# Optimization experiments

Measured on AMD Instinct MI355X. Metric: run time of the kernel, lower is better.

## Reference

```python
import jax, jax.numpy as jnp
import numpy as np
import math

B, S, E, H = 8, 1024, 512, 8
EPS = 1e-5

def _ln(x, g, b):
    mu = jnp.mean(x, axis=-1, keepdims=True)
    var = jnp.mean(jnp.square(x - mu), axis=-1, keepdims=True)
    return (x - mu) * jax.lax.rsqrt(var + EPS) * g + b

def setup_inputs() -> dict:
    key = jax.random.key(0)
    ks = iter(jax.random.split(key, 40))
    def w(shape, scale=0.02):
        return jax.random.normal(next(ks), shape, dtype=jnp.float32) * scale
    inp = {
        'x': jax.random.normal(next(ks), (B, S, E), dtype=jnp.float32),
        'cond': jax.random.normal(next(ks), (B, 1, E), dtype=jnp.float32),
        # AdaLN modulation linears (stored as (in,out))
        'g1w': w((E, E)), 'g1b': jnp.zeros((E,), jnp.float32),
        'be1w': w((E, E)), 'be1b': jnp.zeros((E,), jnp.float32),
        'a1w': w((E, E)), 'a1b': jnp.zeros((E,), jnp.float32),
        'g2w': w((E, E)), 'g2b': jnp.zeros((E,), jnp.float32),
        'be2w': w((E, E)), 'be2b': jnp.zeros((E,), jnp.float32),
        'a2w': w((E, E)), 'a2b': jnp.zeros((E,), jnp.float32),
        # LayerNorm affine
        'ln1g': jnp.ones((E,), jnp.float32), 'ln1b': jnp.zeros((E,), jnp.float32),
        'ln2g': jnp.ones((E,), jnp.float32), 'ln2b': jnp.zeros((E,), jnp.float32),
        # attention projections: each head has width E -> out dim H*E
        'wq': w((E, H * E)), 'bq': jnp.zeros((H * E,), jnp.float32),
        'wk': w((E, H * E)), 'bk': jnp.zeros((H * E,), jnp.float32),
        'wv': w((E, H * E)), 'bv': jnp.zeros((H * E,), jnp.float32),
        'lvw': w((H * E, E)), 'lvb': jnp.zeros((E,), jnp.float32),
        # FFN
        'f1w': w((E, 4 * E)), 'f1b': jnp.zeros((4 * E,), jnp.float32),
        'f2w': w((4 * E, E)), 'f2b': jnp.zeros((E,), jnp.float32),
    }
    return inp

def reference(x, cond, g1w, g1b, be1w, be1b, a1w, a1b, g2w, g2b, be2w, be2b, a2w, a2b,
              ln1g, ln1b, ln2g, ln2b, wq, bq, wk, bk, wv, bv, lvw, lvb, f1w, f1b, f2w, f2b):
    # AdaLN modulation signals, each (B,1,E)
    gamma1 = cond @ g1w + g1b
    beta1 = cond @ be1w + be1b
    alpha1 = cond @ a1w + a1b
    gamma2 = cond @ g2w + g2b
    beta2 = cond @ be2w + be2b
    alpha2 = cond @ a2w + a2b

    y = _ln(x, ln1g, ln1b) * (1.0 + gamma1) + beta1
    q = (y @ wq + bq).reshape(B, S, H, E).transpose(0, 2, 1, 3)  # (B,H,S,E)
    k = (y @ wk + bk).reshape(B, S, H, E).transpose(0, 2, 1, 3)
    v = (y @ wv + bv).reshape(B, S, H, E).transpose(0, 2, 1, 3)
    # NOTE: original scales by sqrt(q.size(2)) == sqrt(seq_len), not head_dim
    scale = 1.0 / math.sqrt(S)
    attn = jax.nn.softmax(jnp.einsum('bhse,bhte->bhst', q, k) * scale, axis=-1)
    o = jnp.einsum('bhst,bhte->bhse', attn, v)  # (B,H,S,E)
    o = o.transpose(0, 2, 1, 3).reshape(B, S, H * E)
    y = x + (o @ lvw + lvb) * alpha1

    z = _ln(y, ln2g, ln2b) * (1.0 + gamma2) + beta2
    z = (jax.nn.relu(z @ f1w + f1b) @ f2w + f2b) * alpha2
    return y + z
```

## Files before the change

### kernel.cpp

```cpp
#include <hip/hip_runtime.h>
#include <hip/hip_bf16.h>

typedef __bf16 bf16_t;
typedef bf16_t bf16x8 __attribute__((ext_vector_type(8)));
typedef bf16_t bf16x4 __attribute__((ext_vector_type(4)));
typedef float f32x4 __attribute__((ext_vector_type(4)));

typedef const __attribute__((address_space(1))) void GV;
typedef __attribute__((address_space(3))) void LV;

__device__ __forceinline__ void gload_lds16(const bf16_t* gsrc, bf16_t* ldst) {
    __builtin_amdgcn_global_load_lds((GV*)gsrc, (LV*)ldst, 16, 0, 0);
}

__global__ __launch_bounds__(256) void wtrans_kernel(const float* __restrict__ in,
                                                     bf16_t* __restrict__ out, int K, int N)
{
    __shared__ float tile[32][33];
    const int n0 = blockIdx.x * 32, k0 = blockIdx.y * 32;
    const int tx = threadIdx.x & 31, ty = threadIdx.x >> 5;
#pragma unroll
    for (int i = 0; i < 32; i += 8)
        tile[ty + i][tx] = in[(long long)(k0 + ty + i) * N + n0 + tx];
    __syncthreads();
#pragma unroll
    for (int i = 0; i < 32; i += 8)
        out[(long long)(n0 + ty + i) * K + k0 + tx] = (bf16_t)tile[tx][ty + i];
}

__global__ __launch_bounds__(256) void modsig_kernel(
    const float* __restrict__ cond,
    const float* __restrict__ w0, const float* __restrict__ w1, const float* __restrict__ w2,
    const float* __restrict__ w3, const float* __restrict__ w4, const float* __restrict__ w5,
    const float* __restrict__ c0, const float* __restrict__ c1, const float* __restrict__ c2,
    const float* __restrict__ c3, const float* __restrict__ c4, const float* __restrict__ c5,
    float* __restrict__ out)
{
    __shared__ float cs[512];
    const int sig = blockIdx.x >> 3, b = blockIdx.x & 7;
    const float* w; const float* bi;
    switch (sig) {
        case 0: w = w0; bi = c0; break;
        case 1: w = w1; bi = c1; break;
        case 2: w = w2; bi = c2; break;
        case 3: w = w3; bi = c3; break;
        case 4: w = w4; bi = c4; break;
        default: w = w5; bi = c5; break;
    }
    for (int i = threadIdx.x; i < 512; i += 256) cs[i] = cond[b * 512 + i];
    __syncthreads();
    for (int n = threadIdx.x; n < 512; n += 256) {
        float s = bi[n];
        for (int i = 0; i < 512; ++i) s = fmaf(cs[i], w[(long long)i * 512 + n], s);
        out[(long long)(sig * 8 + b) * 512 + n] = s;
    }
}

__global__ __launch_bounds__(128) void ln_mod_kernel(
    const float* __restrict__ x, const float* __restrict__ g, const float* __restrict__ be,
    const float* __restrict__ gamma, const float* __restrict__ beta, bf16_t* __restrict__ out)
{
    const int row = blockIdx.x;
    const int b = row >> 10;
    const int t = threadIdx.x;
    const float4 v = reinterpret_cast<const float4*>(x + (long long)row * 512)[t];
    float s = v.x + v.y + v.z + v.w;
    float ss = v.x * v.x + v.y * v.y + v.z * v.z + v.w * v.w;
    for (int o = 32; o; o >>= 1) { s += __shfl_xor(s, o); ss += __shfl_xor(ss, o); }
    __shared__ float red[4];
    if ((t & 63) == 0) { red[t >> 6] = s; red[2 + (t >> 6)] = ss; }
    __syncthreads();
    s = red[0] + red[1]; ss = red[2] + red[3];
    const float mu = s * (1.f / 512.f);
    const float rstd = rsqrtf(ss * (1.f / 512.f) - mu * mu + 1e-5f);
    const float4 gv = reinterpret_cast<const float4*>(g)[t];
    const float4 bv = reinterpret_cast<const float4*>(be)[t];
    const float4 ga = reinterpret_cast<const float4*>(gamma + b * 512)[t];
    const float4 bb = reinterpret_cast<const float4*>(beta + b * 512)[t];
    bf16x4 ov;
    ov[0] = (bf16_t)(((v.x - mu) * rstd * gv.x + bv.x) * (1.f + ga.x) + bb.x);
    ov[1] = (bf16_t)(((v.y - mu) * rstd * gv.y + bv.y) * (1.f + ga.y) + bb.y);
    ov[2] = (bf16_t)(((v.z - mu) * rstd * gv.z + bv.z) * (1.f + ga.z) + bb.z);
    ov[3] = (bf16_t)(((v.w - mu) * rstd * gv.w + bv.w) * (1.f + ga.w) + bb.w);
    reinterpret_cast<bf16x4*>(out + (long long)row * 512)[t] = ov;
}

template <int EPI>
__global__ __launch_bounds__(256) void gemm128_kernel(
    const bf16_t* __restrict__ A, const bf16_t* __restrict__ B,
    const float* __restrict__ bias, void* Cout,
    int M, int N, int K, int lda, int ldb, int ldc)
{
    const int nbx = gridDim.x;
    const int lin = blockIdx.y * nbx + blockIdx.x;
    const int cpx = (nbx * gridDim.y) >> 3;
    const int swz = (lin & 7) * cpx + (lin >> 3);
    const int m0 = (swz / nbx) * 128, n0 = (swz % nbx) * 128;
    const int tid = threadIdx.x, lane = tid & 63, wid = tid >> 6;
    const int wr = wid >> 1, wc = wid & 1;

    __shared__ bf16_t As[8192];
    __shared__ bf16_t Bs[8192];

    f32x4 acc[4][4];
#pragma unroll
    for (int m = 0; m < 4; ++m)
#pragma unroll
        for (int n = 0; n < 4; ++n) acc[m][n] = (f32x4){0.f, 0.f, 0.f, 0.f};

    const int r8 = lane >> 3;
    const int lc = (lane & 7) ^ r8;
    long long aOff[4], bOff[4];
#pragma unroll
    for (int i = 0; i < 4; ++i) {
        const int row = i * 32 + wid * 8 + r8;
        aOff[i] = (long long)(m0 + row) * lda + lc * 8;
        bOff[i] = (long long)(n0 + row) * ldb + lc * 8;
    }

    const int frow = lane & 15, lg = lane >> 4;
    const int p0 = lg ^ (frow & 7);

    for (int kt = 0; kt < K; kt += 64) {
#pragma unroll
        for (int i = 0; i < 4; ++i) gload_lds16(A + aOff[i] + kt, As + i * 2048 + wid * 512);
#pragma unroll
        for (int i = 0; i < 4; ++i) gload_lds16(B + bOff[i] + kt, Bs + i * 2048 + wid * 512);
        __syncthreads();
        __builtin_amdgcn_s_setprio(1);
#pragma unroll
        for (int kk = 0; kk < 2; ++kk) {
            const int pc = p0 ^ (kk << 2);
            bf16x8 af[4], bfv[4];
#pragma unroll
            for (int m = 0; m < 4; ++m)
                af[m] = *reinterpret_cast<const bf16x8*>(As + (wr * 64 + m * 16 + frow) * 64 + pc * 8);
#pragma unroll
            for (int n = 0; n < 4; ++n)
                bfv[n] = *reinterpret_cast<const bf16x8*>(Bs + (wc * 64 + n * 16 + frow) * 64 + pc * 8);
#pragma unroll
            for (int m = 0; m < 4; ++m)
#pragma unroll
                for (int n = 0; n < 4; ++n)
                    acc[m][n] = __builtin_amdgcn_mfma_f32_16x16x32_bf16(af[m], bfv[n], acc[m][n], 0, 0, 0);
        }
        __builtin_amdgcn_s_setprio(0);
        __syncthreads();
    }

#pragma unroll
    for (int m = 0; m < 4; ++m) {
        const int gm = m0 + wr * 64 + m * 16 + ((lane >> 4) << 2);
#pragma unroll
        for (int n = 0; n < 4; ++n) {
            const int gn = n0 + wc * 64 + n * 16 + (lane & 15);
            const float bb = bias ? bias[gn] : 0.f;
#pragma unroll
            for (int j = 0; j < 4; ++j) {
                const float v = acc[m][n][j] + bb;
                const int gmj = gm + j;
                if (EPI == 0) {
                    ((bf16_t*)Cout)[(long long)gmj * ldc + gn] = (bf16_t)v;
                } else {
                    ((bf16_t*)Cout)[(long long)gmj * ldc + gn] = (bf16_t)fmaxf(v, 0.f);
                }
            }
        }
    }
}

__global__ __launch_bounds__(256) void gemmqkv_kernel(
    const bf16_t* __restrict__ A, const bf16_t* __restrict__ B,
    const float* __restrict__ bq, const float* __restrict__ bk, const float* __restrict__ bv,
    bf16_t* __restrict__ qkv, bf16_t* __restrict__ vtb)
{
    const int lin = blockIdx.y * 96 + blockIdx.x;
    const int swz = (lin & 7) * 768 + (lin >> 3);
    const int m0 = (swz / 96) * 128, n0 = (swz % 96) * 128;
    const int sec = n0 >> 12;
    const float* bias = (sec == 0) ? bq : ((sec == 1) ? bk : bv);
    const int tid = threadIdx.x, lane = tid & 63, wid = tid >> 6;
    const int wr = wid >> 1, wc = wid & 1;

    __shared__ bf16_t As[8192];
    __shared__ bf16_t Bs[8192];

    f32x4 acc[4][4];
#pragma unroll
    for (int m = 0; m < 4; ++m)
#pragma unroll
        for (int n = 0; n < 4; ++n) acc[m][n] = (f32x4){0.f, 0.f, 0.f, 0.f};

    const int r8 = lane >> 3;
    const int lc = (lane & 7) ^ r8;
    long long aOff[4], bOff[4];
#pragma unroll
    for (int i = 0; i < 4; ++i) {
        const int row = i * 32 + wid * 8 + r8;
        aOff[i] = (long long)(m0 + row) * 512 + lc * 8;
        bOff[i] = (long long)(n0 + row) * 512 + lc * 8;
    }

    const int frow = lane & 15, lg = lane >> 4;
    const int p0 = lg ^ (frow & 7);

    for (int kt = 0; kt < 512; kt += 64) {
#pragma unroll
        for (int i = 0; i < 4; ++i) gload_lds16(A + aOff[i] + kt, As + i * 2048 + wid * 512);
#pragma unroll
        for (int i = 0; i < 4; ++i) gload_lds16(B + bOff[i] + kt, Bs + i * 2048 + wid * 512);
        __syncthreads();
        __builtin_amdgcn_s_setprio(1);
#pragma unroll
        for (int kk = 0; kk < 2; ++kk) {
            const int pc = p0 ^ (kk << 2);
            bf16x8 af[4], bfv[4];
#pragma unroll
            for (int m = 0; m < 4; ++m)
                af[m] = *reinterpret_cast<const bf16x8*>(As + (wr * 64 + m * 16 + frow) * 64 + pc * 8);
#pragma unroll
            for (int n = 0; n < 4; ++n)
                bfv[n] = *reinterpret_cast<const bf16x8*>(Bs + (wc * 64 + n * 16 + frow) * 64 + pc * 8);
#pragma unroll
            for (int m = 0; m < 4; ++m)
#pragma unroll
                for (int n = 0; n < 4; ++n)
                    acc[m][n] = __builtin_amdgcn_mfma_f32_16x16x32_bf16(af[m], bfv[n], acc[m][n], 0, 0, 0);
        }
        __builtin_amdgcn_s_setprio(0);
        __syncthreads();
    }

#pragma unroll
    for (int m = 0; m < 4; ++m) {
        const int gm = m0 + wr * 64 + m * 16 + ((lane >> 4) << 2);
#pragma unroll
        for (int n = 0; n < 4; ++n) {
            const int gn = n0 + wc * 64 + n * 16 + (lane & 15);
            const int gnl = gn & 4095;
            const float bb = bias[gnl];
#pragma unroll
            for (int j = 0; j < 4; ++j) {
                const float v = acc[m][n][j] + bb;
                const int gmj = gm + j;
                if (sec < 2) {
                    qkv[(long long)sec * 33554432 + (long long)gmj * 4096 + gnl] = (bf16_t)v;
                } else {
                    const long long ci =
                        (long long)(((gmj >> 10) * 8 + (gnl >> 9)) * 512 + (gnl & 511)) * 1024 + (gmj & 1023);
                    vtb[ci] = (bf16_t)v;
                }
            }
        }
    }
}

__global__ __launch_bounds__(256) void gemm64_kernel(
    const bf16_t* __restrict__ A, const bf16_t* __restrict__ B,
    const float* __restrict__ bias, float* __restrict__ Cout,
    const float* __restrict__ resid, const float* __restrict__ alpha,
    int M, int N, int K, int lda, int ldb)
{
    const int nbx = gridDim.x;
    const int lin = blockIdx.y * nbx + blockIdx.x;
    const int cpx = (nbx * gridDim.y) >> 3;
    const int swz = (lin & 7) * cpx + (lin >> 3);
    const int m0 = (swz / nbx) * 64, n0 = (swz % nbx) * 128;
    const int tid = threadIdx.x, lane = tid & 63, wid = tid >> 6;
    const int wr = wid >> 1, wc = wid & 1;

    __shared__ bf16_t As[4096];
    __shared__ bf16_t Bs[8192];

    f32x4 acc[2][4];
#pragma unroll
    for (int m = 0; m < 2; ++m)
#pragma unroll
        for (int n = 0; n < 4; ++n) acc[m][n] = (f32x4){0.f, 0.f, 0.f, 0.f};

    const int r8 = lane >> 3;
    const int lc = (lane & 7) ^ r8;
    long long aOff[2], bOff[4];
#pragma unroll
    for (int i = 0; i < 2; ++i)
        aOff[i] = (long long)(m0 + i * 32 + wid * 8 + r8) * lda + lc * 8;
#pragma unroll
    for (int i = 0; i < 4; ++i)
        bOff[i] = (long long)(n0 + i * 32 + wid * 8 + r8) * ldb + lc * 8;

    const int frow = lane & 15, lg = lane >> 4;
    const int p0 = lg ^ (frow & 7);

    for (int kt = 0; kt < K; kt += 64) {
#pragma unroll
        for (int i = 0; i < 2; ++i) gload_lds16(A + aOff[i] + kt, As + i * 2048 + wid * 512);
#pragma unroll
        for (int i = 0; i < 4; ++i) gload_lds16(B + bOff[i] + kt, Bs + i * 2048 + wid * 512);
        __syncthreads();
        __builtin_amdgcn_s_setprio(1);
#pragma unroll
        for (int kk = 0; kk < 2; ++kk) {
            const int pc = p0 ^ (kk << 2);
            bf16x8 af[2], bfv[4];
#pragma unroll
            for (int m = 0; m < 2; ++m)
                af[m] = *reinterpret_cast<const bf16x8*>(As + (wr * 32 + m * 16 + frow) * 64 + pc * 8);
#pragma unroll
            for (int n = 0; n < 4; ++n)
                bfv[n] = *reinterpret_cast<const bf16x8*>(Bs + (wc * 64 + n * 16 + frow) * 64 + pc * 8);
#pragma unroll
            for (int m = 0; m < 2; ++m)
#pragma unroll
                for (int n = 0; n < 4; ++n)
                    acc[m][n] = __builtin_amdgcn_mfma_f32_16x16x32_bf16(af[m], bfv[n], acc[m][n], 0, 0, 0);
        }
        __builtin_amdgcn_s_setprio(0);
        __syncthreads();
    }

#pragma unroll
    for (int m = 0; m < 2; ++m) {
        const int gm = m0 + wr * 32 + m * 16 + ((lane >> 4) << 2);
#pragma unroll
        for (int n = 0; n < 4; ++n) {
            const int gn = n0 + wc * 64 + n * 16 + (lane & 15);
            const float bb = bias[gn];
#pragma unroll
            for (int j = 0; j < 4; ++j) {
                const int gmj = gm + j;
                const long long ci = (long long)gmj * 512 + gn;
                Cout[ci] = resid[ci] + (acc[m][n][j] + bb) * alpha[(gmj >> 10) * 512 + gn];
            }
        }
    }
}

#define FA_LDS 141312
#define SCL 0.04508422132207354f
__global__ __launch_bounds__(512, 2) void flash_kernel(
    bf16_t* __restrict__ qb, const bf16_t* __restrict__ kb, const bf16_t* __restrict__ vtb)
{
    extern __shared__ char smem[];
    bf16_t* Ks = (bf16_t*)smem;
    bf16_t* Vs = (bf16_t*)(smem + 65536);
    char* PB = smem + 131072;
    float* pmaxB = (float*)(smem + 139264);
    float* psumB = (float*)(smem + 140288);

    const int bid = blockIdx.x;
    const int xcd = bid & 7, idx = bid >> 3;
    const int qt = idx & 15, bhl = idx >> 4;
    const int bh = xcd * 8 + bhl;
    const int b = bh >> 3, h = bh & 7;
    const int q0 = qt * 64;
    const int tid = threadIdx.x, lane = tid & 63, wid = tid >> 6;
    const int laneq = lane & 15, lx = lane & 7, lg = lane >> 4;
    const int wk = wid >> 2, wq = wid & 3;
    const int we = wid & 3, wq2 = wid >> 2;

#pragma unroll
    for (int r = 0; r < 8; ++r) {
        const int row = r * 8 + wid;
        gload_lds16(kb + ((long long)(b * 1024 + row) * 8 + h) * 512 + ((lane ^ (row & 7)) << 3),
                    Ks + row * 512);
    }
    const int qi = wq * 16 + laneq;
    bf16x8 qfrag[16];
    {
        const bf16_t* qrow = qb + ((long long)(b * 1024 + q0 + qi) * 8 + h) * 512 + lg * 8;
#pragma unroll
        for (int ks = 0; ks < 16; ++ks) qfrag[ks] = *reinterpret_cast<const bf16x8*>(qrow + ks * 32);
    }
    f32x4 accA[8], accB[8];
#pragma unroll
    for (int e = 0; e < 8; ++e) { accA[e] = (f32x4){0.f,0.f,0.f,0.f}; accB[e] = (f32x4){0.f,0.f,0.f,0.f}; }
    float mS = 0.f, mPA = 0.f, mPB = 0.f, lA = 0.f, lB = 0.f;
    const int rA0 = wk * 32 + laneq, rA1 = rA0 + 16;
    const int qA = wq2 * 32 + laneq, qB = qA + 16;
    const int qx = (qi & 7) << 1;
    const int qxA = (qA & 7) << 1, qxB = (qB & 7) << 1;
    __syncthreads();

    for (int t = 0; t < 16; ++t) {
        const int kv0 = t * 64;
#pragma unroll
        for (int r = 0; r < 8; ++r) {
            const int e = r * 64 + wid * 8 + (lane >> 3);
            gload_lds16(vtb + ((long long)bh * 512 + e) * 1024 + kv0 + ((lx ^ (e & 7)) << 3),
                        Vs + (r * 64 + wid * 8) * 64);
        }
        f32x4 s0 = (f32x4){0.f,0.f,0.f,0.f}, s1 = (f32x4){0.f,0.f,0.f,0.f};
        const char* KsB = (const char*)Ks;
        __builtin_amdgcn_s_setprio(1);
#pragma unroll
        for (int ks = 0; ks < 16; ++ks) {
            const int co = ((ks * 4 + lg) ^ lx) << 4;
            bf16x8 a0 = *(const bf16x8*)(KsB + rA0 * 1024 + co);
            bf16x8 a1 = *(const bf16x8*)(KsB + rA1 * 1024 + co);
            s0 = __builtin_amdgcn_mfma_f32_16x16x32_bf16(a0, qfrag[ks], s0, 0, 0, 0);
            s1 = __builtin_amdgcn_mfma_f32_16x16x32_bf16(a1, qfrag[ks], s1, 0, 0, 0);
        }
        __builtin_amdgcn_s_setprio(0);
        float f[8];
#pragma unroll
        for (int j = 0; j < 4; ++j) { f[j] = s0[j] * SCL; f[4 + j] = s1[j] * SCL; }
        float mloc = f[0];
#pragma unroll
        for (int j = 1; j < 8; ++j) mloc = fmaxf(mloc, f[j]);
        mloc = fmaxf(mloc, __shfl_xor(mloc, 16));
        mloc = fmaxf(mloc, __shfl_xor(mloc, 32));
        float pe[8]; float sl = 0.f;
#pragma unroll
        for (int j = 0; j < 8; ++j) { pe[j] = exp2f(f[j] - mS); sl += pe[j]; }
        sl += __shfl_xor(sl, 16);
        sl += __shfl_xor(sl, 32);
        if (lane < 16) {
            pmaxB[(t & 1) * 128 + wk * 64 + wq * 16 + lane] = mloc;
            psumB[(t & 1) * 128 + wk * 64 + wq * 16 + lane] = sl;
        }
        {
            bf16x4 p0, p1;
#pragma unroll
            for (int j = 0; j < 4; ++j) { p0[j] = (bf16_t)pe[j]; p1[j] = (bf16_t)pe[4 + j]; }
            const int kc0 = wk * 8 + lg, kc1 = kc0 + 4;
            *(bf16x4*)(PB + qi * 128 + ((kc0 ^ qx) << 3)) = p0;
            *(bf16x4*)(PB + qi * 128 + ((kc1 ^ qx) << 3)) = p1;
        }
        __syncthreads();

        if (t < 15) {
#pragma unroll
            for (int r = 0; r < 8; ++r) {
                const int row = r * 8 + wid;
                gload_lds16(kb + ((long long)(b * 1024 + kv0 + 64 + row) * 8 + h) * 512
                                + ((lane ^ (row & 7)) << 3),
                            Ks + row * 512);
            }
        }
        const char* VB = (const char*)Vs;
        __builtin_amdgcn_s_setprio(1);
#pragma unroll
        for (int ks2 = 0; ks2 < 2; ++ks2) {
            const int kcp = ks2 * 8 + lg * 2;
            bf16x8 pA = *(const bf16x8*)(PB + qA * 128 + ((kcp ^ qxA) << 3));
            bf16x8 pBv = *(const bf16x8*)(PB + qB * 128 + ((kcp ^ qxB) << 3));
            const int kcv = ks2 * 4 + lg;
#pragma unroll
            for (int ef = 0; ef < 8; ++ef) {
                const int re = we * 128 + ef * 16 + laneq;
                bf16x8 av = *(const bf16x8*)(VB + re * 128 + ((kcv ^ lx) << 4));
                accA[ef] = __builtin_amdgcn_mfma_f32_16x16x32_bf16(av, pA, accA[ef], 0, 0, 0);
                accB[ef] = __builtin_amdgcn_mfma_f32_16x16x32_bf16(av, pBv, accB[ef], 0, 0, 0);
            }
        }
        __builtin_amdgcn_s_setprio(0);
        {
            const float* pmax_t = pmaxB + (t & 1) * 128;
            const float* psum_t = psumB + (t & 1) * 128;
            mS = fmaxf(mS, fmaxf(pmax_t[qi], pmax_t[64 + qi]));
            lA += psum_t[qA] + psum_t[64 + qA];
            lB += psum_t[qB] + psum_t[64 + qB];
            const float mnA = fmaxf(mPA, fmaxf(pmax_t[qA], pmax_t[64 + qA]));
            const float mnB = fmaxf(mPB, fmaxf(pmax_t[qB], pmax_t[64 + qB]));
            if (__ballot((mnA > mPA) || (mnB > mPB))) {
                const float rA = exp2f(mPA - mnA), rB = exp2f(mPB - mnB);
                lA *= rA; lB *= rB;
#pragma unroll
                for (int e = 0; e < 8; ++e) {
#pragma unroll
                    for (int j = 0; j < 4; ++j) { accA[e][j] *= rA; accB[e][j] *= rB; }
                }
            }
            mPA = mnA; mPB = mnB;
        }
        __syncthreads();
    }

    const float iA = 1.f / lA, iB = 1.f / lB;
#pragma unroll
    for (int ef = 0; ef < 8; ++ef) {
        const int e0 = we * 128 + ef * 16 + lg * 4;
        bf16x4 oA, oB;
#pragma unroll
        for (int j = 0; j < 4; ++j) { oA[j] = (bf16_t)(accA[ef][j] * iA); oB[j] = (bf16_t)(accB[ef][j] * iB); }
        *(bf16x4*)(qb + ((long long)(b * 1024 + q0 + qA) * 8 + h) * 512 + e0) = oA;
        *(bf16x4*)(qb + ((long long)(b * 1024 + q0 + qB) * 8 + h) * 512 + e0) = oB;
    }
}

extern "C" void kernel_launch(void* const* d_in, const int* in_sizes, int n_in,
                              void* d_out, int out_size, void* d_ws, size_t ws_size,
                              hipStream_t stream)
{
    const float* x    = (const float*)d_in[0];
    const float* cond = (const float*)d_in[1];
    const float* g1w  = (const float*)d_in[2];  const float* g1b  = (const float*)d_in[3];
    const float* be1w = (const float*)d_in[4];  const float* be1b = (const float*)d_in[5];
    const float* a1w  = (const float*)d_in[6];  const float* a1b  = (const float*)d_in[7];
    const float* g2w  = (const float*)d_in[8];  const float* g2b  = (const float*)d_in[9];
    const float* be2w = (const float*)d_in[10]; const float* be2b = (const float*)d_in[11];
    const float* a2w  = (const float*)d_in[12]; const float* a2b  = (const float*)d_in[13];
    const float* ln1g = (const float*)d_in[14]; const float* ln1b = (const float*)d_in[15];
    const float* ln2g = (const float*)d_in[16]; const float* ln2b = (const float*)d_in[17];
    const float* wq   = (const float*)d_in[18]; const float* bq   = (const float*)d_in[19];
    const float* wk   = (const float*)d_in[20]; const float* bk   = (const float*)d_in[21];
    const float* wv   = (const float*)d_in[22]; const float* bv   = (const float*)d_in[23];
    const float* lvw  = (const float*)d_in[24]; const float* lvb  = (const float*)d_in[25];
    const float* f1w  = (const float*)d_in[26]; const float* f1b  = (const float*)d_in[27];
    const float* f2w  = (const float*)d_in[28]; const float* f2b  = (const float*)d_in[29];
    (void)in_sizes; (void)n_in; (void)out_size; (void)ws_size;

    char* w8 = (char*)d_ws;
    float*  mod  = (float*)(w8);
    bf16_t* wqT  = (bf16_t*)(w8 + 98304);
    bf16_t* lvwT = (bf16_t*)(w8 + 98304 + 3 * 4194304);
    bf16_t* f1wT = (bf16_t*)(w8 + 98304 + 4 * 4194304);
    bf16_t* f2wT = (bf16_t*)(w8 + 98304 + 4 * 4194304 + 2097152);
    bf16_t* ybf  = (bf16_t*)(w8 + 98304 + 4 * 4194304 + 2 * 2097152);
    bf16_t* qb   = (bf16_t*)(w8 + 98304 + 4 * 4194304 + 2 * 2097152 + 8388608);
    bf16_t* kb   = qb + 33554432;
    bf16_t* vtb  = kb + 33554432;

    (void)hipFuncSetAttribute((const void*)flash_kernel,
                              hipFuncAttributeMaxDynamicSharedMemorySize, FA_LDS);

    const dim3 blk(256);
    wtrans_kernel<<<dim3(128, 16), blk, 0, stream>>>(wq, wqT, 512, 4096);
    wtrans_kernel<<<dim3(128, 16), blk, 0, stream>>>(wk, wqT + 2097152, 512, 4096);
    wtrans_kernel<<<dim3(128, 16), blk, 0, stream>>>(wv, wqT + 2 * 2097152, 512, 4096);
    wtrans_kernel<<<dim3(16, 128), blk, 0, stream>>>(lvw, lvwT, 4096, 512);
    wtrans_kernel<<<dim3(64, 16), blk, 0, stream>>>(f1w, f1wT, 512, 2048);
    wtrans_kernel<<<dim3(16, 64), blk, 0, stream>>>(f2w, f2wT, 2048, 512);
    modsig_kernel<<<48, blk, 0, stream>>>(cond, g1w, be1w, a1w, g2w, be2w, a2w,
                                          g1b, be1b, a1b, g2b, be2b, a2b, mod);
    ln_mod_kernel<<<8192, 128, 0, stream>>>(x, ln1g, ln1b, mod, mod + 4096, ybf);
    gemmqkv_kernel<<<dim3(96, 64), blk, 0, stream>>>(ybf, wqT, bq, bk, bv, qb, vtb);
    flash_kernel<<<1024, 512, FA_LDS, stream>>>(qb, kb, vtb);
    gemm64_kernel<<<dim3(4, 128), blk, 0, stream>>>(qb, lvwT, lvb, (float*)d_out, x, mod + 8192,
        8192, 512, 4096, 4096, 4096);
    ln_mod_kernel<<<8192, 128, 0, stream>>>((const float*)d_out, ln2g, ln2b,
                                            mod + 12288, mod + 16384, ybf);
    gemm128_kernel<1><<<dim3(16, 64), blk, 0, stream>>>(ybf, f1wT, f1b, qb,
        8192, 2048, 512, 512, 512, 2048);
    gemm64_kernel<<<dim3(4, 128), blk, 0, stream>>>(qb, f2wT, f2b, (float*)d_out,
        (const float*)d_out, mod + 20480,
        8192, 512, 2048, 2048, 2048);
}
```

Baseline: 691.6 us.

## Shrink flash attention tiles to 32 queries and 32 keys with 256-thread blocks

Restructures the flash-attention kernel to handle 32 query rows per block with 32-key KV tiles, using 4 waves instead of 8 and halving LDS to about 67 KB. The grid doubles to 2048 blocks and the K/V/P swizzles are reworked for the narrower tiles. The aim is higher occupancy and more blocks per CU to hide latency. In exchange, each block reloads the full K and V for its fewer query rows, doubling K/V global traffic, and runs twice as many loop iterations with barriers.

After: 675.8 us. 2.3% less time.

```diff
diff --git a/kernel.cpp b/kernel.cpp
--- a/kernel.cpp
+++ b/kernel.cpp
@@ -335,32 +335,32 @@
     }
 }
 
-#define FA_LDS 141312
+#define FA_LDS 68608
 #define SCL 0.04508422132207354f
-__global__ __launch_bounds__(512, 2) void flash_kernel(
+__global__ __launch_bounds__(256, 2) void flash_kernel(
     bf16_t* __restrict__ qb, const bf16_t* __restrict__ kb, const bf16_t* __restrict__ vtb)
 {
     extern __shared__ char smem[];
     bf16_t* Ks = (bf16_t*)smem;
-    bf16_t* Vs = (bf16_t*)(smem + 65536);
-    char* PB = smem + 131072;
-    float* pmaxB = (float*)(smem + 139264);
-    float* psumB = (float*)(smem + 140288);
+    bf16_t* Vs = (bf16_t*)(smem + 32768);
+    char* PB = smem + 65536;
+    float* pmaxB = (float*)(smem + 67584);
+    float* psumB = (float*)(smem + 68096);
 
     const int bid = blockIdx.x;
     const int xcd = bid & 7, idx = bid >> 3;
-    const int qt = idx & 15, bhl = idx >> 4;
+    const int qt = idx & 31, bhl = idx >> 5;
     const int bh = xcd * 8 + bhl;
     const int b = bh >> 3, h = bh & 7;
-    const int q0 = qt * 64;
+    const int q0 = qt * 32;
     const int tid = threadIdx.x, lane = tid & 63, wid = tid >> 6;
     const int laneq = lane & 15, lx = lane & 7, lg = lane >> 4;
-    const int wk = wid >> 2, wq = wid & 3;
-    const int we = wid & 3, wq2 = wid >> 2;
+    const int wk = wid >> 1, wq = wid & 1;
+    const int we = wid;
 
 #pragma unroll
     for (int r = 0; r < 8; ++r) {
-        const int row = r * 8 + wid;
+        const int row = r * 4 + wid;
         gload_lds16(kb + ((long long)(b * 1024 + row) * 8 + h) * 512 + ((lane ^ (row & 7)) << 3),
                     Ks + row * 512);
     }
@@ -375,100 +375,88 @@
 #pragma unroll
     for (int e = 0; e < 8; ++e) { accA[e] = (f32x4){0.f,0.f,0.f,0.f}; accB[e] = (f32x4){0.f,0.f,0.f,0.f}; }
     float mS = 0.f, mPA = 0.f, mPB = 0.f, lA = 0.f, lB = 0.f;
-    const int rA0 = wk * 32 + laneq, rA1 = rA0 + 16;
-    const int qA = wq2 * 32 + laneq, qB = qA + 16;
-    const int qx = (qi & 7) << 1;
-    const int qxA = (qA & 7) << 1, qxB = (qB & 7) << 1;
+    const int rA = wk * 16 + laneq;
+    const int qA = laneq, qB = laneq + 16;
     __syncthreads();
 
-    for (int t = 0; t < 16; ++t) {
-        const int kv0 = t * 64;
+    for (int t = 0; t < 32; ++t) {
 #pragma unroll
         for (int r = 0; r < 8; ++r) {
-            const int e = r * 64 + wid * 8 + (lane >> 3);
-            gload_lds16(vtb + ((long long)bh * 512 + e) * 1024 + kv0 + ((lx ^ (e & 7)) << 3),
-                        Vs + (r * 64 + wid * 8) * 64);
-        }
-        f32x4 s0 = (f32x4){0.f,0.f,0.f,0.f}, s1 = (f32x4){0.f,0.f,0.f,0.f};
+            const int e0 = (r * 4 + wid) * 16;
+            const int e = e0 + (lane >> 2);
+            gload_lds16(vtb + ((long long)bh * 512 + e) * 1024 + t * 32 + (((lane & 3) ^ (e & 3)) << 3),
+                        Vs + e0 * 32);
+        }
+        f32x4 s0 = (f32x4){0.f, 0.f, 0.f, 0.f};
         const char* KsB = (const char*)Ks;
         __builtin_amdgcn_s_setprio(1);
 #pragma unroll
         for (int ks = 0; ks < 16; ++ks) {
-            const int co = ((ks * 4 + lg) ^ lx) << 4;
-            bf16x8 a0 = *(const bf16x8*)(KsB + rA0 * 1024 + co);
-            bf16x8 a1 = *(const bf16x8*)(KsB + rA1 * 1024 + co);
+            const int co = (((ks * 4 + lg) ^ lx) << 4);
+            bf16x8 a0 = *(const bf16x8*)(KsB + rA * 1024 + co);
             s0 = __builtin_amdgcn_mfma_f32_16x16x32_bf16(a0, qfrag[ks], s0, 0, 0, 0);
-            s1 = __builtin_amdgcn_mfma_f32_16x16x32_bf16(a1, qfrag[ks], s1, 0, 0, 0);
         }
         __builtin_amdgcn_s_setprio(0);
-        float f[8];
-#pragma unroll
-        for (int j = 0; j < 4; ++j) { f[j] = s0[j] * SCL; f[4 + j] = s1[j] * SCL; }
-        float mloc = f[0];
-#pragma unroll
-        for (int j = 1; j < 8; ++j) mloc = fmaxf(mloc, f[j]);
+        float f[4], pe[4];
+#pragma unroll
+        for (int j = 0; j < 4; ++j) f[j] = s0[j] * SCL;
+        float mloc = fmaxf(fmaxf(f[0], f[1]), fmaxf(f[2], f[3]));
         mloc = fmaxf(mloc, __shfl_xor(mloc, 16));
         mloc = fmaxf(mloc, __shfl_xor(mloc, 32));
-        float pe[8]; float sl = 0.f;
-#pragma unroll
-        for (int j = 0; j < 8; ++j) { pe[j] = exp2f(f[j] - mS); sl += pe[j]; }
+        float sl = 0.f;
+#pragma unroll
+        for (int j = 0; j < 4; ++j) { pe[j] = exp2f(f[j] - mS); sl += pe[j]; }
         sl += __shfl_xor(sl, 16);
         sl += __shfl_xor(sl, 32);
         if (lane < 16) {
-            pmaxB[(t & 1) * 128 + wk * 64 + wq * 16 + lane] = mloc;
-            psumB[(t & 1) * 128 + wk * 64 + wq * 16 + lane] = sl;
+            pmaxB[(t & 1) * 64 + wk * 32 + wq * 16 + lane] = mloc;
+            psumB[(t & 1) * 64 + wk * 32 + wq * 16 + lane] = sl;
         }
         {
-            bf16x4 p0, p1;
-#pragma unroll
-            for (int j = 0; j < 4; ++j) { p0[j] = (bf16_t)pe[j]; p1[j] = (bf16_t)pe[4 + j]; }
-            const int kc0 = wk * 8 + lg, kc1 = kc0 + 4;
-            *(bf16x4*)(PB + qi * 128 + ((kc0 ^ qx) << 3)) = p0;
-            *(bf16x4*)(PB + qi * 128 + ((kc1 ^ qx) << 3)) = p1;
-        }
-        __syncthreads();
-
-        if (t < 15) {
+            bf16x4 p;
+#pragma unroll
+            for (int j = 0; j < 4; ++j) p[j] = (bf16_t)pe[j];
+            const int g = wk * 4 + lg;
+            *(bf16x4*)(PB + qi * 64 + (((g >> 1) ^ (qi & 3)) << 4) + ((g & 1) << 3)) = p;
+        }
+        __syncthreads();
+
+        if (t < 31) {
 #pragma unroll
             for (int r = 0; r < 8; ++r) {
-                const int row = r * 8 + wid;
-                gload_lds16(kb + ((long long)(b * 1024 + kv0 + 64 + row) * 8 + h) * 512
+                const int row = r * 4 + wid;
+                gload_lds16(kb + ((long long)(b * 1024 + t * 32 + 32 + row) * 8 + h) * 512
                                 + ((lane ^ (row & 7)) << 3),
                             Ks + row * 512);
             }
         }
         const char* VB = (const char*)Vs;
+        bf16x8 pA = *(const bf16x8*)(PB + qA * 64 + ((lg ^ (qA & 3)) << 4));
+        bf16x8 pBv = *(const bf16x8*)(PB + qB * 64 + ((lg ^ (qB & 3)) << 4));
         __builtin_amdgcn_s_setprio(1);
 #pragma unroll
-        for (int ks2 = 0; ks2 < 2; ++ks2) {
-            const int kcp = ks2 * 8 + lg * 2;
-            bf16x8 pA = *(const bf16x8*)(PB + qA * 128 + ((kcp ^ qxA) << 3));
-            bf16x8 pBv = *(const bf16x8*)(PB + qB * 128 + ((kcp ^ qxB) << 3));
-            const int kcv = ks2 * 4 + lg;
-#pragma unroll
-            for (int ef = 0; ef < 8; ++ef) {
-                const int re = we * 128 + ef * 16 + laneq;
-                bf16x8 av = *(const bf16x8*)(VB + re * 128 + ((kcv ^ lx) << 4));
-                accA[ef] = __builtin_amdgcn_mfma_f32_16x16x32_bf16(av, pA, accA[ef], 0, 0, 0);
-                accB[ef] = __builtin_amdgcn_mfma_f32_16x16x32_bf16(av, pBv, accB[ef], 0, 0, 0);
-            }
+        for (int ef = 0; ef < 8; ++ef) {
+            const int re = we * 128 + ef * 16 + laneq;
+            bf16x8 av = *(const bf16x8*)(VB + re * 64 + ((lg ^ (re & 3)) << 4));
+            accA[ef] = __builtin_amdgcn_mfma_f32_16x16x32_bf16(av, pA, accA[ef], 0, 0, 0);
+            accB[ef] = __builtin_amdgcn_mfma_f32_16x16x32_bf16(av, pBv, accB[ef], 0, 0, 0);
         }
         __builtin_amdgcn_s_setprio(0);
         {
-            const float* pmax_t = pmaxB + (t & 1) * 128;
-            const float* psum_t = psumB + (t & 1) * 128;
-            mS = fmaxf(mS, fmaxf(pmax_t[qi], pmax_t[64 + qi]));
-            lA += psum_t[qA] + psum_t[64 + qA];
-            lB += psum_t[qB] + psum_t[64 + qB];
-            const float mnA = fmaxf(mPA, fmaxf(pmax_t[qA], pmax_t[64 + qA]));
-            const float mnB = fmaxf(mPB, fmaxf(pmax_t[qB], pmax_t[64 + qB]));
+            const float* pmax_t = pmaxB + (t & 1) * 64;
+            const float* psum_t = psumB + (t & 1) * 64;
+            mS = fmaxf(mS, fmaxf(pmax_t[qi], pmax_t[32 + qi]));
+            lA += psum_t[qA] + psum_t[32 + qA];
+            lB += psum_t[qB] + psum_t[32 + qB];
+            const float mnA = fmaxf(mPA, fmaxf(pmax_t[qA], pmax_t[32 + qA]));
+            const float mnB = fmaxf(mPB, fmaxf(pmax_t[qB], pmax_t[32 + qB]));
             if (__ballot((mnA > mPA) || (mnB > mPB))) {
-                const float rA = exp2f(mPA - mnA), rB = exp2f(mPB - mnB);
-                lA *= rA; lB *= rB;
+                const float rsA = exp2f(mPA - mnA), rsB = exp2f(mPB - mnB);
+                lA *= rsA; lB *= rsB;
 #pragma unroll
                 for (int e = 0; e < 8; ++e) {
 #pragma unroll
-                    for (int j = 0; j < 4; ++j) { accA[e][j] *= rA; accB[e][j] *= rB; }
+                    for (int j = 0; j < 4; ++j) { accA[e][j] *= rsA; accB[e][j] *= rsB; }
                 }
             }
             mPA = mnA; mPB = mnB;
@@ -535,7 +523,7 @@
                                           g1b, be1b, a1b, g2b, be2b, a2b, mod);
     ln_mod_kernel<<<8192, 128, 0, stream>>>(x, ln1g, ln1b, mod, mod + 4096, ybf);
     gemmqkv_kernel<<<dim3(96, 64), blk, 0, stream>>>(ybf, wqT, bq, bk, bv, qb, vtb);
-    flash_kernel<<<1024, 512, FA_LDS, stream>>>(qb, kb, vtb);
+    flash_kernel<<<2048, 256, FA_LDS, stream>>>(qb, kb, vtb);
     gemm64_kernel<<<dim3(4, 128), blk, 0, stream>>>(qb, lvwT, lvb, (float*)d_out, x, mod + 8192,
         8192, 512, 4096, 4096, 4096);
     ln_mod_kernel<<<8192, 128, 0, stream>>>((const float*)d_out, ln2g, ln2b,
```
